# Performance work log

Measured on AMD Instinct MI355X. Metric: run time of the kernel, lower is better.

The kernel has to match this reference:

```python
import jax, jax.numpy as jnp
import numpy as np

TWO_PI = 2.0 * np.pi


def interp_H_circular(coords, signal):
    """Circular linear interpolation over a uniform group grid.
    coords: [M, 1] angles; signal: [K, C]. Returns [M, C]."""
    K = signal.shape[0]
    step = TWO_PI / K
    t = jnp.mod(coords[:, 0], TWO_PI) / step          # [M]
    i0f = jnp.floor(t)
    frac = (t - i0f)[:, None]                          # [M, 1]
    i0 = i0f.astype(jnp.int32) % K
    i1 = (i0 + 1) % K
    return (1.0 - frac) * signal[i0] + frac * signal[i1]


def rotate_grid(angles, grid):
    """angles: [No]; grid: [ks, ks, 2] (x, y). Returns [No, ks, ks, 2]."""
    c, s = jnp.cos(angles), jnp.sin(angles)
    R = jnp.stack([jnp.stack([c, -s], -1), jnp.stack([s, c], -1)], -2)  # [No,2,2]
    return jnp.einsum('nij,hwj->nhwi', R, grid)


def bilinear_sample(img, grid):
    """img: [B, H, W]; grid: [B, h, w, 2] with (x, y) in [-1, 1].
    Zero padding outside, align_corners-style mapping. Returns [B, h, w]."""
    B, H, W = img.shape
    x = (grid[..., 0] + 1.0) * 0.5 * (W - 1)
    y = (grid[..., 1] + 1.0) * 0.5 * (H - 1)
    x0f, y0f = jnp.floor(x), jnp.floor(y)
    wx, wy = x - x0f, y - y0f
    x0, y0 = x0f.astype(jnp.int32), y0f.astype(jnp.int32)
    b = jnp.arange(B)[:, None, None]

    def gather(yy, xx):
        valid = (yy >= 0) & (yy < H) & (xx >= 0) & (xx < W)
        v = img[b, jnp.clip(yy, 0, H - 1), jnp.clip(xx, 0, W - 1)]
        return jnp.where(valid, v, 0.0)

    return ((1 - wy) * (1 - wx) * gather(y0, x0)
            + (1 - wy) * wx * gather(y0, x0 + 1)
            + wy * (1 - wx) * gather(y0 + 1, x0)
            + wy * wx * gather(y0 + 1, x0 + 1))


def setup_inputs() -> dict:
    key = jax.random.key(0)
    k1, k2, k3, k4 = jax.random.split(key, 4)
    O, CIN, K, KS, NI, NO = 512, 512, 16, 7, 16, 16
    in_H = jax.random.uniform(k1, (NI, 1), dtype=jnp.float32) * TWO_PI
    out_H = jax.random.uniform(k2, (NO, 1), dtype=jnp.float32) * TWO_PI
    weight_H = jax.random.normal(k3, (O, CIN, K), dtype=jnp.float32) * 0.05
    weight = jax.random.normal(k4, (O, 1, KS, KS), dtype=jnp.float32) * 0.05
    grid_H = (jnp.arange(K, dtype=jnp.float32) * (TWO_PI / K)).reshape(K, 1)
    lin = jnp.linspace(-1.0, 1.0, KS, dtype=jnp.float32)
    gx, gy = jnp.meshgrid(lin, lin, indexing='xy')
    grid_Rn = jnp.stack([gx, gy], axis=-1)  # [KS, KS, 2]
    mask = jnp.ones((KS, KS), dtype=jnp.float32)
    return {"in_H": in_H, "out_H": out_H, "weight_H": weight_H,
            "weight": weight, "grid_H": grid_H, "grid_Rn": grid_Rn,
            "mask": mask}


def reference(in_H, out_H, weight_H, weight, grid_H, grid_Rn, mask):
    NI, NO = in_H.shape[0], out_H.shape[0]
    O, CIN_G, K = weight_H.shape
    KS = weight.shape[-1]

    out_H_inv = -out_H                                            # inverse_H
    # left_apply_to_H: pairwise group product -> [NI, NO, 1]
    H_prod_H = jnp.mod(in_H[:, None, :] + out_H_inv[None, :, :], TWO_PI)
    # left_apply_to_Rn: rotate spatial grid -> [NO, KS, KS, 2]
    H_prod_Rn = rotate_grid(out_H_inv[:, 0], grid_Rn)

    # interpolate_H over group grid of signal [K, CIN_G*O]
    sig = jnp.transpose(weight_H, (2, 1, 0)).reshape(K, -1)
    wH = interp_H_circular(H_prod_H.reshape(-1, 1), sig)          # [NI*NO, CIN_G*O]
    wH = wH.reshape(NI, NO, CIN_G, O)
    # .transpose(0,3).transpose(1,3) == permutation (3,0,2,1)
    weight_H_out = jnp.transpose(wH, (3, 0, 2, 1))                # [O, NI, CIN_G, NO]

    # interpolate_Rn: repeat_interleave kernels, tile rotated grids
    imgs = jnp.repeat(weight[:, 0], NO, axis=0)                   # [O*NO, KS, KS]
    grids = jnp.tile(H_prod_Rn, (O, 1, 1, 1))                     # [O*NO, KS, KS, 2]
    w = bilinear_sample(imgs, grids).reshape(O, NO, 1, KS, KS)
    w = mask * w                                                  # broadcast mask
    return (weight_H_out, w)
```

## Files before the change

kernel.cpp:

```cpp
#include <hip/hip_runtime.h>

#define TWO_PI_F 6.283185307179586f

#define C_O   512
#define C_CIN 512
#define C_K   16
#define C_KS  7
#define C_NI  16
#define C_NO  16

#define OUT0_SIZE (C_O * C_NI * C_CIN * C_NO)
#define OUT1_SIZE (C_O * C_NO * C_KS * C_KS)

#define SW_STRIDE 18

#define BILIN_BLOCKS  784
#define INTERP_BLOCKS 4096

typedef float f32x4 __attribute__((ext_vector_type(4)));

__global__ __launch_bounds__(512, 8) void fused_kernel(
    const float* __restrict__ in_H,
    const float* __restrict__ out_H,
    const float* __restrict__ weight_H,
    const float* __restrict__ weight,
    const float* __restrict__ grid_Rn,
    const float* __restrict__ mask,
    float* __restrict__ out0,
    float* __restrict__ out1)
{
    __shared__ float s_w[256 * SW_STRIDE];
    __shared__ float s_t[64];

    const int tid = threadIdx.x;
    const int bid = blockIdx.x;

    if (bid < BILIN_BLOCKS) {
        int idx = bid * 512 + tid;
        int pix = idx % 49;
        int no  = (idx / 49) & 15;
        int o   = idx / (49 * 16);

        float gx = grid_Rn[pix * 2 + 0];
        float gy = grid_Rn[pix * 2 + 1];

        float ang = -out_H[no];
        float sn, cs;
        sincosf(ang, &sn, &cs);

        float x = cs * gx - sn * gy;
        float y = sn * gx + cs * gy;

        float X = (x + 1.0f) * 3.0f;
        float Y = (y + 1.0f) * 3.0f;

        float x0f = floorf(X), y0f = floorf(Y);
        float wx = X - x0f,    wy = Y - y0f;
        int   x0 = (int)x0f,   y0 = (int)y0f;

        const float* img = weight + o * 49;

        auto gat = [&](int yy, int xx) -> float {
            bool v = (yy >= 0) & (yy < 7) & (xx >= 0) & (xx < 7);
            int yc = min(max(yy, 0), 6);
            int xc = min(max(xx, 0), 6);
            float val = img[yc * 7 + xc];
            return v ? val : 0.0f;
        };

        float r = (1.0f - wy) * (1.0f - wx) * gat(y0,     x0)
                + (1.0f - wy) * wx          * gat(y0,     x0 + 1)
                + wy          * (1.0f - wx) * gat(y0 + 1, x0)
                + wy          * wx          * gat(y0 + 1, x0 + 1);

        out1[idx] = mask[pix] * r;
        return;
    }

    const int ibid = bid - BILIN_BLOCKS;
    const int o    = ibid >> 3;
    const int ch   = (ibid >> 2) & 1;
    const int nig  = ibid & 3;

    if (tid < 64) {
        int ni_l = tid >> 4;
        int no   = tid & 15;
        float x = in_H[nig * 4 + ni_l] - out_H[no];
        float r = fmodf(x, TWO_PI_F);
        if (r < 0.0f) r += TWO_PI_F;
        s_t[tid] = r * (16.0f / TWO_PI_F);
    }

    const float4* wsrc = reinterpret_cast<const float4*>(weight_H)
                       + (size_t)o * 2048 + ch * 1024;
#pragma unroll
    for (int j = 0; j < 2; ++j) {
        int f = j * 512 + tid;
        float4 v = wsrc[f];
        int c    = f >> 2;
        int part = f & 3;
        float* row = &s_w[c * SW_STRIDE + part * 4];
        reinterpret_cast<float2*>(row)[0] = make_float2(v.x, v.y);
        reinterpret_cast<float2*>(row)[1] = make_float2(v.z, v.w);
        if (part == 0) s_w[c * SW_STRIDE + 16] = v.x;
    }
    __syncthreads();

    const int q    = tid & 3;
    const int crow = tid >> 2;
    f32x4* obase = reinterpret_cast<f32x4*>(out0)
                 + ((size_t)((o << 4) + (nig << 2)) << 11) + (ch << 10);

#pragma unroll
    for (int ni_l = 0; ni_l < 4; ++ni_l) {
        int   i0e[4];
        float fe[4];
#pragma unroll
        for (int e = 0; e < 4; ++e) {
            float tt = s_t[ni_l * 16 + q * 4 + e];
            float fl = floorf(tt);
            i0e[e] = ((int)fl) & 15;
            fe[e]  = tt - fl;
        }
#pragma unroll
        for (int half = 0; half < 2; ++half) {
            const float* wv = &s_w[(half * 128 + crow) * SW_STRIDE];
            f32x4 res;
            res.x = (1.0f - fe[0]) * wv[i0e[0]] + fe[0] * wv[i0e[0] + 1];
            res.y = (1.0f - fe[1]) * wv[i0e[1]] + fe[1] * wv[i0e[1] + 1];
            res.z = (1.0f - fe[2]) * wv[i0e[2]] + fe[2] * wv[i0e[2] + 1];
            res.w = (1.0f - fe[3]) * wv[i0e[3]] + fe[3] * wv[i0e[3] + 1];
            obase[ni_l * 2048 + half * 512 + tid] = res;
        }
    }
}

extern "C" void kernel_launch(void* const* d_in, const int* in_sizes, int n_in,
                              void* d_out, int out_size, void* d_ws, size_t ws_size,
                              hipStream_t stream) {
    const float* in_H     = (const float*)d_in[0];
    const float* out_H    = (const float*)d_in[1];
    const float* weight_H = (const float*)d_in[2];
    const float* weight   = (const float*)d_in[3];
    const float* grid_Rn  = (const float*)d_in[5];
    const float* mask     = (const float*)d_in[6];

    float* out0 = (float*)d_out;
    float* out1 = out0 + OUT0_SIZE;

    hipLaunchKernelGGL(fused_kernel, dim3(BILIN_BLOCKS + INTERP_BLOCKS), dim3(512),
                       0, stream,
                       in_H, out_H, weight_H, weight, grid_Rn, mask, out0, out1);
}
```

Before: 55.02 us.

## Fold bilinear sampling work into interp blocks and pair output stores

Removes the 784 dedicated bilinear-sampling blocks and instead spreads that work across all 4096 interpolation blocks, with 98 threads per block each computing one output pixel after their interpolation stores. The interpolation loop is also restructured to compute two ni slices at once, so four 16-byte stores are issued together per iteration. This cuts the total block count and launch imbalance, at the cost of extra tail work with divergent lanes in every block. It also adds register pressure from the paired computation.

```diff
diff --git a/kernel.cpp b/kernel.cpp
--- a/kernel.cpp
+++ b/kernel.cpp
@@ -14,8 +14,8 @@
 
 #define SW_STRIDE 18
 
-#define BILIN_BLOCKS  784
-#define INTERP_BLOCKS 4096
+#define NBLOCKS 4096
+#define BILIN_PER_BLOCK 98
 
 typedef float f32x4 __attribute__((ext_vector_type(4)));
 
@@ -35,52 +35,9 @@
     const int tid = threadIdx.x;
     const int bid = blockIdx.x;
 
-    if (bid < BILIN_BLOCKS) {
-        int idx = bid * 512 + tid;
-        int pix = idx % 49;
-        int no  = (idx / 49) & 15;
-        int o   = idx / (49 * 16);
-
-        float gx = grid_Rn[pix * 2 + 0];
-        float gy = grid_Rn[pix * 2 + 1];
-
-        float ang = -out_H[no];
-        float sn, cs;
-        sincosf(ang, &sn, &cs);
-
-        float x = cs * gx - sn * gy;
-        float y = sn * gx + cs * gy;
-
-        float X = (x + 1.0f) * 3.0f;
-        float Y = (y + 1.0f) * 3.0f;
-
-        float x0f = floorf(X), y0f = floorf(Y);
-        float wx = X - x0f,    wy = Y - y0f;
-        int   x0 = (int)x0f,   y0 = (int)y0f;
-
-        const float* img = weight + o * 49;
-
-        auto gat = [&](int yy, int xx) -> float {
-            bool v = (yy >= 0) & (yy < 7) & (xx >= 0) & (xx < 7);
-            int yc = min(max(yy, 0), 6);
-            int xc = min(max(xx, 0), 6);
-            float val = img[yc * 7 + xc];
-            return v ? val : 0.0f;
-        };
-
-        float r = (1.0f - wy) * (1.0f - wx) * gat(y0,     x0)
-                + (1.0f - wy) * wx          * gat(y0,     x0 + 1)
-                + wy          * (1.0f - wx) * gat(y0 + 1, x0)
-                + wy          * wx          * gat(y0 + 1, x0 + 1);
-
-        out1[idx] = mask[pix] * r;
-        return;
-    }
-
-    const int ibid = bid - BILIN_BLOCKS;
-    const int o    = ibid >> 3;
-    const int ch   = (ibid >> 2) & 1;
-    const int nig  = ibid & 3;
+    const int o   = bid >> 3;
+    const int ch  = (bid >> 2) & 1;
+    const int nig = bid & 3;
 
     if (tid < 64) {
         int ni_l = tid >> 4;
@@ -108,30 +65,86 @@
 
     const int q    = tid & 3;
     const int crow = tid >> 2;
+    const float* wv0 = &s_w[crow * SW_STRIDE];
+    const float* wv1 = &s_w[(128 + crow) * SW_STRIDE];
     f32x4* obase = reinterpret_cast<f32x4*>(out0)
-                 + ((size_t)((o << 4) + (nig << 2)) << 11) + (ch << 10);
+                 + ((size_t)((o << 4) + (nig << 2)) << 11) + (ch << 10) + tid;
 
 #pragma unroll
-    for (int ni_l = 0; ni_l < 4; ++ni_l) {
-        int   i0e[4];
-        float fe[4];
+    for (int pair = 0; pair < 2; ++pair) {
+        int   i0a[4], i0b[4];
+        float fa[4],  fb[4];
 #pragma unroll
         for (int e = 0; e < 4; ++e) {
-            float tt = s_t[ni_l * 16 + q * 4 + e];
-            float fl = floorf(tt);
-            i0e[e] = ((int)fl) & 15;
-            fe[e]  = tt - fl;
+            float ta = s_t[(pair * 2 + 0) * 16 + q * 4 + e];
+            float fl = floorf(ta);
+            i0a[e] = ((int)fl) & 15;  fa[e] = ta - fl;
+            float tb = s_t[(pair * 2 + 1) * 16 + q * 4 + e];
+            float fl2 = floorf(tb);
+            i0b[e] = ((int)fl2) & 15; fb[e] = tb - fl2;
         }
-#pragma unroll
-        for (int half = 0; half < 2; ++half) {
-            const float* wv = &s_w[(half * 128 + crow) * SW_STRIDE];
-            f32x4 res;
-            res.x = (1.0f - fe[0]) * wv[i0e[0]] + fe[0] * wv[i0e[0] + 1];
-            res.y = (1.0f - fe[1]) * wv[i0e[1]] + fe[1] * wv[i0e[1] + 1];
-            res.z = (1.0f - fe[2]) * wv[i0e[2]] + fe[2] * wv[i0e[2] + 1];
-            res.w = (1.0f - fe[3]) * wv[i0e[3]] + fe[3] * wv[i0e[3] + 1];
-            obase[ni_l * 2048 + half * 512 + tid] = res;
-        }
+        f32x4 r00, r01, r10, r11;
+        r00.x = (1.0f - fa[0]) * wv0[i0a[0]] + fa[0] * wv0[i0a[0] + 1];
+        r00.y = (1.0f - fa[1]) * wv0[i0a[1]] + fa[1] * wv0[i0a[1] + 1];
+        r00.z = (1.0f - fa[2]) * wv0[i0a[2]] + fa[2] * wv0[i0a[2] + 1];
+        r00.w = (1.0f - fa[3]) * wv0[i0a[3]] + fa[3] * wv0[i0a[3] + 1];
+        r01.x = (1.0f - fa[0]) * wv1[i0a[0]] + fa[0] * wv1[i0a[0] + 1];
+        r01.y = (1.0f - fa[1]) * wv1[i0a[1]] + fa[1] * wv1[i0a[1] + 1];
+        r01.z = (1.0f - fa[2]) * wv1[i0a[2]] + fa[2] * wv1[i0a[2] + 1];
+        r01.w = (1.0f - fa[3]) * wv1[i0a[3]] + fa[3] * wv1[i0a[3] + 1];
+        r10.x = (1.0f - fb[0]) * wv0[i0b[0]] + fb[0] * wv0[i0b[0] + 1];
+        r10.y = (1.0f - fb[1]) * wv0[i0b[1]] + fb[1] * wv0[i0b[1] + 1];
+        r10.z = (1.0f - fb[2]) * wv0[i0b[2]] + fb[2] * wv0[i0b[2] + 1];
+        r10.w = (1.0f - fb[3]) * wv0[i0b[3]] + fb[3] * wv0[i0b[3] + 1];
+        r11.x = (1.0f - fb[0]) * wv1[i0b[0]] + fb[0] * wv1[i0b[0] + 1];
+        r11.y = (1.0f - fb[1]) * wv1[i0b[1]] + fb[1] * wv1[i0b[1] + 1];
+        r11.z = (1.0f - fb[2]) * wv1[i0b[2]] + fb[2] * wv1[i0b[2] + 1];
+        r11.w = (1.0f - fb[3]) * wv1[i0b[3]] + fb[3] * wv1[i0b[3] + 1];
+        obase[(pair * 2 + 0) * 2048      ] = r00;
+        obase[(pair * 2 + 0) * 2048 + 512] = r01;
+        obase[(pair * 2 + 1) * 2048      ] = r10;
+        obase[(pair * 2 + 1) * 2048 + 512] = r11;
+    }
+
+    if (tid < BILIN_PER_BLOCK) {
+        int idx = bid * BILIN_PER_BLOCK + tid;
+        int pix = idx % 49;
+        int no  = (idx / 49) & 15;
+        int oo  = idx / (49 * 16);
+
+        float gx = grid_Rn[pix * 2 + 0];
+        float gy = grid_Rn[pix * 2 + 1];
+
+        float ang = -out_H[no];
+        float sn, cs;
+        sincosf(ang, &sn, &cs);
+
+        float x = cs * gx - sn * gy;
+        float y = sn * gx + cs * gy;
+
+        float X = (x + 1.0f) * 3.0f;
+        float Y = (y + 1.0f) * 3.0f;
+
+        float x0f = floorf(X), y0f = floorf(Y);
+        float wx = X - x0f,    wy = Y - y0f;
+        int   x0 = (int)x0f,   y0 = (int)y0f;
+
+        const float* img = weight + oo * 49;
+
+        auto gat = [&](int yy, int xx) -> float {
+            bool v = (yy >= 0) & (yy < 7) & (xx >= 0) & (xx < 7);
+            int yc = min(max(yy, 0), 6);
+            int xc = min(max(xx, 0), 6);
+            float val = img[yc * 7 + xc];
+            return v ? val : 0.0f;
+        };
+
+        float r = (1.0f - wy) * (1.0f - wx) * gat(y0,     x0)
+                + (1.0f - wy) * wx          * gat(y0,     x0 + 1)
+                + wy          * (1.0f - wx) * gat(y0 + 1, x0)
+                + wy          * wx          * gat(y0 + 1, x0 + 1);
+
+        out1[idx] = mask[pix] * r;
     }
 }
 
@@ -148,7 +161,6 @@
     float* out0 = (float*)d_out;
     float* out1 = out0 + OUT0_SIZE;
 
-    hipLaunchKernelGGL(fused_kernel, dim3(BILIN_BLOCKS + INTERP_BLOCKS), dim3(512),
-                       0, stream,
+    hipLaunchKernelGGL(fused_kernel, dim3(NBLOCKS), dim3(512), 0, stream,
                        in_H, out_H, weight_H, weight, grid_Rn, mask, out0, out1);
 }
```

Result: no change. 55.88 us (+1.6%).
